# Kernel optimization log

Hardware: AMD Instinct MI355X
Metric: run time of the kernel (lower is better)

Reference implementation:

```python
import jax, jax.numpy as jnp
import numpy as np

B, P, C, UP = 4, 512, 384, 4
K1, K2, KR = 16, 8, 16
NOISE_SCALE = 0.02


def setup_inputs() -> dict:
    key = jax.random.key(0)
    ks = jax.random.split(key, 32)
    w = lambda i, s: (jax.random.normal(ks[i], s, jnp.float32) * 0.02)
    return {
        "ctx_xyz": jax.random.normal(ks[0], (B, P, 3), jnp.float32),
        "ctx_tokens": jax.random.normal(ks[1], (B, P, C), jnp.float32),
        "pred_xyz": jax.random.normal(ks[2], (B, P, 3), jnp.float32),
        "pred_token": jax.random.normal(ks[3], (B, P, C), jnp.float32),
        "noise": jax.random.normal(ks[4], (B, P * UP, 3), jnp.float32),
        "conv1_w1": w(5, (2 * C, C // 2)), "conv1_b1": jnp.zeros((C // 2,), jnp.float32),
        "conv1_w2": w(6, (C // 2, C // 2)), "conv1_b2": jnp.zeros((C // 2,), jnp.float32),
        "conv2_w1": w(7, (2 * (C // 2), C // 4)), "conv2_b1": jnp.zeros((C // 4,), jnp.float32),
        "conv2_w2": w(8, (C // 4, C // 4)), "conv2_b2": jnp.zeros((C // 4,), jnp.float32),
        "cdef_w1": w(9, (C // 4, C // 4)), "cdef_b1": jnp.zeros((C // 4,), jnp.float32),
        "cdef_w2": w(10, (C // 4, 3)), "cdef_b2": jnp.zeros((3,), jnp.float32),
        "fold_w1": w(11, (C // 4 + 3, 256)), "fold_b1": jnp.zeros((256,), jnp.float32),
        "fold_w2": w(12, (256, 256)), "fold_b2": jnp.zeros((256,), jnp.float32),
        "fold_w3": w(13, (256, 3)), "fold_b3": jnp.zeros((3,), jnp.float32),
        "ref_w1": w(14, (2 * (C // 4 + 3), C)), "ref_b1": jnp.zeros((C,), jnp.float32),
        "ref_w2": w(15, (C, 3)), "ref_b2": jnp.zeros((3,), jnp.float32),
    }


def knn_idx(x, k):
    # x: [N, D]; k nearest neighbors by L2, no self-loops (as knn_graph loop=False)
    sq = jnp.sum(x * x, axis=1)
    d = sq[:, None] + sq[None, :] - 2.0 * (x @ x.T)  # [N, N]
    n = x.shape[0]
    d = d.at[jnp.arange(n), jnp.arange(n)].set(jnp.inf)
    return jax.lax.top_k(-d, k)[1]  # [N, k]


def edge_max(x, idx, mlp):
    # EdgeConv: out[i] = max_j mlp([x_i, x_j - x_i])
    n, k = idx.shape
    xi = jnp.broadcast_to(x[:, None, :], (n, k, x.shape[1]))
    xj = x[idx]  # [N, k, D]
    return jnp.max(mlp(jnp.concatenate([xi, xj - xi], axis=-1)), axis=1)


def mlp2(w1, b1, w2, b2):
    return lambda t: jnp.maximum(t @ w1 + b1, 0.0) @ w2 + b2


def reference(ctx_xyz, ctx_tokens, pred_xyz, pred_token, noise,
              conv1_w1, conv1_b1, conv1_w2, conv1_b2,
              conv2_w1, conv2_b1, conv2_w2, conv2_b2,
              cdef_w1, cdef_b1, cdef_w2, cdef_b2,
              fold_w1, fold_b1, fold_w2, fold_b2, fold_w3, fold_b3,
              ref_w1, ref_b1, ref_w2, ref_b2):
    def shared_edgeconv(x):
        h = edge_max(x, knn_idx(x, K1), mlp2(conv1_w1, conv1_b1, conv1_w2, conv1_b2))
        return edge_max(h, knn_idx(h, K2), mlp2(conv2_w1, conv2_b1, conv2_w2, conv2_b2))

    # context branch
    ctx_xyz_f = ctx_xyz.reshape(-1, 3)
    ctx_tok_f = ctx_tokens.reshape(-1, C)
    ctx_feat = shared_edgeconv(ctx_tok_f)                       # [B*P, C//4]
    ctx_xyz_out = ctx_xyz_f + 0.05 * mlp2(cdef_w1, cdef_b1, cdef_w2, cdef_b2)(ctx_feat)

    # target branch: upsample + assign tokens
    tgt_xyz = (jnp.repeat(pred_xyz, UP, axis=1) + NOISE_SCALE * noise).reshape(-1, 3)
    tgt_tok = jnp.repeat(ctx_tokens, UP, axis=1).reshape(-1, C)
    tgt_feat = shared_edgeconv(tgt_tok)                         # [B*P*UP, C//4]

    # folding MLP (Linear-ReLU-Linear-ReLU-Linear) residual
    h = jnp.concatenate([tgt_xyz, tgt_feat], axis=-1)
    h = jnp.maximum(h @ fold_w1 + fold_b1, 0.0)
    h = jnp.maximum(h @ fold_w2 + fold_b2, 0.0)
    tgt_xyz = tgt_xyz + h @ fold_w3 + fold_b3

    # GNN refiner: knn over xyz, EdgeConv over [feat, xyz]
    idx = knn_idx(tgt_xyz, KR)
    xcat = jnp.concatenate([tgt_feat, tgt_xyz], axis=-1)
    tgt_xyz = tgt_xyz + edge_max(xcat, idx, mlp2(ref_w1, ref_b1, ref_w2, ref_b2))

    return jnp.concatenate([ctx_xyz_out, tgt_xyz], axis=0)
```

## Files before the change

### kernel.cpp

```cpp
#include <hip/hip_runtime.h>

#define N2 2048
#define N8 8192
#define CDIM 384
#define H1C 192
#define H2C 96
#define PDIM 512
#define KRR 16
#define FOLDH 256
#define XCAP 256
#define XTILE 1024
#define INFF 3.0e38f

__device__ __forceinline__ float frelu(float x) { return x > 0.f ? x : 0.f; }

__device__ __forceinline__ void bitonic64_val(float& d, int lane) {
    #pragma unroll
    for (int k = 2; k <= 64; k <<= 1) {
        #pragma unroll
        for (int j = k >> 1; j > 0; j >>= 1) {
            float od = __shfl_xor(d, j);
            bool lower = (lane & j) == 0;
            bool olt = od < d;
            bool take = lower ? olt : !olt;
            if (lane & k) take = !take;
            if (take) d = od;
        }
    }
}

__device__ __forceinline__ void bitonic64_pair(float& d, int& c, int lane) {
    #pragma unroll
    for (int k = 2; k <= 64; k <<= 1) {
        #pragma unroll
        for (int j = k >> 1; j > 0; j >>= 1) {
            float od = __shfl_xor(d, j);
            int   oc = __shfl_xor(c, j);
            bool lower = (lane & j) == 0;
            bool olt = (od < d) || (od == d && oc < c);
            bool take = lower ? olt : !olt;
            if (lane & k) take = !take;
            if (take) { d = od; c = oc; }
        }
    }
}

__device__ __forceinline__ void select_slow(const float* bd, const int* bi, int cnt,
                                            int ksel, int row, int n, int* out, int lane) {
    float cd[4]; int cix[4];
    #pragma unroll
    for (int s = 0; s < 4; ++s) {
        int c = lane + 64*s;
        bool v = c < cnt;
        cd[s]  = v ? bd[c] : INFF;
        cix[s] = v ? bi[c] : 0x7fffffff;
    }
    for (int r = 0; r < ksel; ++r) {
        float lv = cd[0]; int li = cix[0];
        #pragma unroll
        for (int s = 1; s < 4; ++s) {
            if (cd[s] < lv || (cd[s] == lv && cix[s] < li)) { lv = cd[s]; li = cix[s]; }
        }
        float wv = lv; int wi = li;
        #pragma unroll
        for (int s = 1; s < 64; s <<= 1) {
            float ov = __shfl_xor(wv, s); int oi = __shfl_xor(wi, s);
            if (ov < wv || (ov == wv && oi < wi)) { wv = ov; wi = oi; }
        }
        if (lane == 0) {
            int safe = ((unsigned)wi < (unsigned)n) ? wi : ((row + 1) & (n - 1));
            out[row*ksel + r] = safe;
        }
        #pragma unroll
        for (int s = 0; s < 4; ++s) {
            if (cd[s] == wv && cix[s] == wi) { cd[s] = INFF; cix[s] = 0x7fffffff; }
        }
    }
}

__global__ __launch_bounds__(256) void rowsq_kernel(const float* __restrict__ x,
                                                    float* __restrict__ sq, int d) {
    int wave = threadIdx.x >> 6, lane = threadIdx.x & 63;
    int row = blockIdx.x*4 + wave;
    float acc = 0.f;
    for (int k = lane; k < d; k += 64) { float v = x[(size_t)row*d + k]; acc += v*v; }
    #pragma unroll
    for (int s = 1; s < 64; s <<= 1) acc += __shfl_xor(acc, s);
    if (lane == 0) sq[row] = acc;
}

__device__ __forceinline__ void disttri_body(const float* __restrict__ x, const float* __restrict__ sq,
                                             float* __restrict__ dist, int n, int K) {
    int l = blockIdx.x;
    int by = (int)((sqrtf(8.f*(float)l + 1.f) - 1.f)*0.5f);
    while ((by+1)*(by+2)/2 <= l) ++by;
    while (by*(by+1)/2 > l) --by;
    int bx = l - by*(by+1)/2;
    int row0 = by*64, col0 = bx*64;
    __shared__ __align__(16) float As[16][68];
    __shared__ __align__(16) float Bs[16][68];
    __shared__ __align__(16) float T[64][68];
    int tx = threadIdx.x, ty = threadIdx.y;
    int t = ty*16 + tx;
    float acc[4][4] = {};
    for (int k0 = 0; k0 < K; k0 += 16) {
        #pragma unroll
        for (int r = 0; r < 4; ++r) {
            int e = t + 256*r; int kk = e & 15, mm = e >> 4;
            As[kk][mm] = x[(size_t)(row0+mm)*K + k0+kk];
            Bs[kk][mm] = x[(size_t)(col0+mm)*K + k0+kk];
        }
        __syncthreads();
        #pragma unroll
        for (int kk = 0; kk < 16; ++kk) {
            float4 a4 = *(const float4*)&As[kk][ty*4];
            float4 b4 = *(const float4*)&Bs[kk][tx*4];
            acc[0][0] += a4.x*b4.x; acc[0][1] += a4.x*b4.y; acc[0][2] += a4.x*b4.z; acc[0][3] += a4.x*b4.w;
            acc[1][0] += a4.y*b4.x; acc[1][1] += a4.y*b4.y; acc[1][2] += a4.y*b4.z; acc[1][3] += a4.y*b4.w;
            acc[2][0] += a4.z*b4.x; acc[2][1] += a4.z*b4.y; acc[2][2] += a4.z*b4.z; acc[2][3] += a4.z*b4.w;
            acc[3][0] += a4.w*b4.x; acc[3][1] += a4.w*b4.y; acc[3][2] += a4.w*b4.z; acc[3][3] += a4.w*b4.w;
        }
        __syncthreads();
    }
    bool mirror = (row0 != col0);
    #pragma unroll
    for (int i2 = 0; i2 < 4; ++i2) {
        int row = row0 + ty*4 + i2;
        float sr = sq[row];
        float4 o;
        o.x = sr + sq[col0+tx*4+0] - 2.f*acc[i2][0];
        o.y = sr + sq[col0+tx*4+1] - 2.f*acc[i2][1];
        o.z = sr + sq[col0+tx*4+2] - 2.f*acc[i2][2];
        o.w = sr + sq[col0+tx*4+3] - 2.f*acc[i2][3];
        *(float4*)&dist[(size_t)row*n + col0 + tx*4] = o;
        if (mirror) {
            T[tx*4+0][ty*4+i2] = o.x;
            T[tx*4+1][ty*4+i2] = o.y;
            T[tx*4+2][ty*4+i2] = o.z;
            T[tx*4+3][ty*4+i2] = o.w;
        }
    }
    if (mirror) {
        __syncthreads();
        #pragma unroll
        for (int i2 = 0; i2 < 4; ++i2) {
            int orow = col0 + ty*4 + i2;
            float4 o = *(const float4*)&T[ty*4+i2][tx*4];
            *(float4*)&dist[(size_t)orow*n + row0 + tx*4] = o;
        }
    }
}

__global__ __launch_bounds__(256) void dist64tri_kernel(const float* __restrict__ x,
                                                        const float* __restrict__ sq,
                                                        float* __restrict__ dist, int n, int K) {
    disttri_body(x, sq, dist, n, K);
}

__global__ __launch_bounds__(256) void distpairtri_kernel(const float* __restrict__ xA,
                                                          const float* __restrict__ sqA,
                                                          float* __restrict__ dA,
                                                          const float* __restrict__ xB,
                                                          const float* __restrict__ sqB,
                                                          float* __restrict__ dB, int n, int K) {
    const float* x  = blockIdx.z ? xB : xA;
    const float* sq = blockIdx.z ? sqB : sqA;
    float* dist     = blockIdx.z ? dB : dA;
    disttri_body(x, sq, dist, n, K);
}

__device__ __forceinline__ void gemm_body(const float* __restrict__ A, const float* __restrict__ Bw,
                                          const float* __restrict__ BwB, const float* __restrict__ bias,
                                          float* __restrict__ C, int m, int K) {
    __shared__ __align__(16) float As[16][68];
    __shared__ __align__(16) float Bs[16][68];
    int tx = threadIdx.x, ty = threadIdx.y;
    int t = ty*16 + tx;
    int row0 = blockIdx.y*64, col0 = blockIdx.x*64;
    float acc[4][4] = {};
    for (int k0 = 0; k0 < K; k0 += 16) {
        #pragma unroll
        for (int r = 0; r < 4; ++r) {
            int e = t + 256*r; int kk = e & 15, mm = e >> 4;
            As[kk][mm] = (k0 + kk < K) ? A[(size_t)(row0+mm)*K + k0+kk] : 0.f;
        }
        #pragma unroll
        for (int r = 0; r < 4; ++r) {
            int e = t + 256*r; int nn = e & 63, kk = e >> 6;
            int col = col0 + nn, k = k0 + kk;
            float bv = 0.f;
            if (k < K && col < m) {
                bv = Bw[(size_t)k*m + col];
                if (BwB) bv -= BwB[(size_t)k*m + col];
            }
            Bs[kk][nn] = bv;
        }
        __syncthreads();
        #pragma unroll
        for (int kk = 0; kk < 16; ++kk) {
            float4 a4 = *(const float4*)&As[kk][ty*4];
            float4 b4 = *(const float4*)&Bs[kk][tx*4];
            acc[0][0] += a4.x*b4.x; acc[0][1] += a4.x*b4.y; acc[0][2] += a4.x*b4.z; acc[0][3] += a4.x*b4.w;
            acc[1][0] += a4.y*b4.x; acc[1][1] += a4.y*b4.y; acc[1][2] += a4.y*b4.z; acc[1][3] += a4.y*b4.w;
            acc[2][0] += a4.z*b4.x; acc[2][1] += a4.z*b4.y; acc[2][2] += a4.z*b4.z; acc[2][3] += a4.z*b4.w;
            acc[3][0] += a4.w*b4.x; acc[3][1] += a4.w*b4.y; acc[3][2] += a4.w*b4.z; acc[3][3] += a4.w*b4.w;
        }
        __syncthreads();
    }
    #pragma unroll
    for (int i2 = 0; i2 < 4; ++i2) {
        int row = row0 + ty*4 + i2;
        #pragma unroll
        for (int j2 = 0; j2 < 4; ++j2) {
            int col = col0 + tx*4 + j2;
            if (col < m) C[(size_t)row*m + col] = acc[i2][j2] + (bias ? bias[col] : 0.f);
        }
    }
}

__global__ __launch_bounds__(256) void gemmquad_kernel(
    const float* A0, const float* Bw0, const float* BwB0, const float* bias0, float* C0,
    const float* A1, const float* Bw1, const float* BwB1, const float* bias1, float* C1,
    const float* A2, const float* Bw2, const float* BwB2, const float* bias2, float* C2,
    const float* A3, const float* Bw3, const float* BwB3, const float* bias3, float* C3,
    int m, int K) {
    int z = blockIdx.z;
    const float* A    = (z==0)?A0 :(z==1)?A1 :(z==2)?A2 :A3;
    const float* Bw   = (z==0)?Bw0:(z==1)?Bw1:(z==2)?Bw2:Bw3;
    const float* BwB  = (z==0)?BwB0:(z==1)?BwB1:(z==2)?BwB2:BwB3;
    const float* bias = (z==0)?bias0:(z==1)?bias1:(z==2)?bias2:bias3;
    float* C          = (z==0)?C0 :(z==1)?C1 :(z==2)?C2 :C3;
    gemm_body(A, Bw, BwB, bias, C, m, K);
}

template<int ETOT, int SELF, int IDXS, int YT>
__device__ __forceinline__ void edge_gemm_body(const float* __restrict__ u, const float* __restrict__ v,
                                               const int* __restrict__ idx,
                                               const float* __restrict__ Bw, const float* __restrict__ bias,
                                               float* __restrict__ O, int m, int K, int npts) {
    if ((int)blockIdx.y >= YT) return;
    __shared__ __align__(16) float As[16][68];
    __shared__ __align__(16) float Bs[16][68];
    int tx = threadIdx.x, ty = threadIdx.y;
    int t = ty*16 + tx;
    int row0 = blockIdx.y*64, col0 = blockIdx.x*64;
    float acc[4][4] = {};
    for (int k0 = 0; k0 < K; k0 += 16) {
        #pragma unroll
        for (int r = 0; r < 4; ++r) {
            int e_ = t + 256*r; int kk = e_ & 15, mm = e_ >> 4;
            int row = row0 + mm, k = k0 + kk;
            int i = row / ETOT;
            int e = row - i*ETOT;
            int j = (SELF && e == 0) ? i : idx[i*IDXS + (e - SELF)];
            j = ((unsigned)j < (unsigned)npts) ? j : i;
            As[kk][mm] = frelu(u[(size_t)i*K + k] + v[(size_t)j*K + k]);
        }
        #pragma unroll
        for (int r = 0; r < 4; ++r) {
            int e_ = t + 256*r; int nn = e_ & 63, kk = e_ >> 6;
            Bs[kk][nn] = Bw[(size_t)(k0+kk)*m + col0 + nn];
        }
        __syncthreads();
        #pragma unroll
        for (int kk = 0; kk < 16; ++kk) {
            float4 a4 = *(const float4*)&As[kk][ty*4];
            float4 b4 = *(const float4*)&Bs[kk][tx*4];
            acc[0][0] += a4.x*b4.x; acc[0][1] += a4.x*b4.y; acc[0][2] += a4.x*b4.z; acc[0][3] += a4.x*b4.w;
            acc[1][0] += a4.y*b4.x; acc[1][1] += a4.y*b4.y; acc[1][2] += a4.y*b4.z; acc[1][3] += a4.y*b4.w;
            acc[2][0] += a4.z*b4.x; acc[2][1] += a4.z*b4.y; acc[2][2] += a4.z*b4.z; acc[2][3] += a4.z*b4.w;
            acc[3][0] += a4.w*b4.x; acc[3][1] += a4.w*b4.y; acc[3][2] += a4.w*b4.z; acc[3][3] += a4.w*b4.w;
        }
        __syncthreads();
    }
    #pragma unroll
    for (int i2 = 0; i2 < 4; ++i2) {
        int row = row0 + ty*4 + i2;
        #pragma unroll
        for (int j2 = 0; j2 < 4; ++j2) {
            int col = col0 + tx*4 + j2;
            O[(size_t)row*m + col] = acc[i2][j2] + bias[col];
        }
    }
}

__global__ __launch_bounds__(256) void edge_gemm1_kernel(const float* u1, const float* v1,
                                                         const int* cidx1,
                                                         const float* Bw, const float* bias,
                                                         float* Octx, float* Otgt, int npts) {
    if (blockIdx.z == 0) edge_gemm_body<16,0,16,512>(u1, v1, cidx1, Bw, bias, Octx, H1C, H1C, npts);
    else                 edge_gemm_body<5,1,16,160>(u1, v1, cidx1, Bw, bias, Otgt, H1C, H1C, npts);
}

__global__ __launch_bounds__(256) void edge_gemm2_kernel(const float* u2c, const float* v2c,
                                                         const float* u2t, const float* v2t,
                                                         const int* cidx2, const int* tidx2,
                                                         const float* Bw, const float* bias,
                                                         float* Octx, float* Otgt, int npts) {
    if (blockIdx.z == 0) edge_gemm_body<8,0,8,256>(u2c, v2c, cidx2, Bw, bias, Octx, H2C, H2C, npts);
    else                 edge_gemm_body<3,1,2,96>(u2t, v2t, tidx2, Bw, bias, Otgt, H2C, H2C, npts);
}

__global__ __launch_bounds__(192) void reduce1_kernel(const float* __restrict__ O1c,
                                                      const float* __restrict__ O1t,
                                                      float* __restrict__ h_ctx, float* __restrict__ sq_c,
                                                      float* __restrict__ h_tgt, float* __restrict__ sq_t) {
    int i = blockIdx.x, tid = threadIdx.x, wave = tid >> 6, lane = tid & 63;
    __shared__ float pm[3];
    const float* O = blockIdx.y ? O1t : O1c;
    float* h   = blockIdx.y ? h_tgt : h_ctx;
    float* sqo = blockIdx.y ? sq_t : sq_c;
    int E = blockIdx.y ? 5 : 16;
    const float* base = O + (size_t)i*E*H1C + tid;
    float best = base[0];
    for (int e = 1; e < E; ++e) best = fmaxf(best, base[(size_t)e*H1C]);
    h[(size_t)i*H1C + tid] = best;
    float part = best*best;
    #pragma unroll
    for (int s = 1; s < 64; s <<= 1) part += __shfl_xor(part, s);
    if (lane == 0) pm[wave] = part;
    __syncthreads();
    if (tid == 0) sqo[i] = pm[0] + pm[1] + pm[2];
}

__global__ __launch_bounds__(128) void reduce2_kernel(const float* __restrict__ O2c,
                                                      const float* __restrict__ O2t,
                                                      const float* __restrict__ cdw1, const float* __restrict__ cdb1,
                                                      const float* __restrict__ cdw2, const float* __restrict__ cdb2,
                                                      const float* __restrict__ ctx_xyz,
                                                      float* __restrict__ out_ctx, float* __restrict__ tfeat) {
    int i = blockIdx.x, tid = threadIdx.x, wave = tid >> 6, lane = tid & 63;
    __shared__ float sf_[96], st2_[96];
    if (blockIdx.y == 1) {
        if (tid < 96) {
            const float* base = O2t + (size_t)i*3*H2C + tid;
            float best = fmaxf(fmaxf(base[0], base[H2C]), base[2*H2C]);
            tfeat[(size_t)i*H2C + tid] = best;
        }
        return;
    }
    if (tid < 96) {
        const float* base = O2c + (size_t)i*8*H2C + tid;
        float best = base[0];
        #pragma unroll
        for (int e = 1; e < 8; ++e) best = fmaxf(best, base[(size_t)e*H2C]);
        sf_[tid] = best;
    }
    __syncthreads();
    if (tid < 96) {
        float a = cdb1[tid];
        for (int k = 0; k < 96; ++k) a += sf_[k]*cdw1[k*96 + tid];
        st2_[tid] = frelu(a);
    }
    __syncthreads();
    if (wave == 0) {
        float s0 = st2_[lane];
        float p0 = s0*cdw2[lane*3+0], p1 = s0*cdw2[lane*3+1], p2 = s0*cdw2[lane*3+2];
        if (lane < 32) {
            float s1 = st2_[lane+64];
            p0 += s1*cdw2[(lane+64)*3+0];
            p1 += s1*cdw2[(lane+64)*3+1];
            p2 += s1*cdw2[(lane+64)*3+2];
        }
        #pragma unroll
        for (int s = 1; s < 64; s <<= 1) {
            p0 += __shfl_xor(p0, s); p1 += __shfl_xor(p1, s); p2 += __shfl_xor(p2, s);
        }
        if (lane == 0) {
            out_ctx[i*3+0] = ctx_xyz[i*3+0] + 0.05f*(cdb2[0] + p0);
            out_ctx[i*3+1] = ctx_xyz[i*3+1] + 0.05f*(cdb2[1] + p1);
            out_ctx[i*3+2] = ctx_xyz[i*3+2] + 0.05f*(cdb2[2] + p2);
        }
    }
}

__global__ __launch_bounds__(256) void gatherpair_kernel(
    const float* __restrict__ featd, const float* __restrict__ xyzg,
    const float* Bw0, const float* BwB0, const float* bias0, float* C0,
    const float* Bw1, const float* BwB1, const float* bias1, float* C1,
    int m, int K) {
    int z = blockIdx.z;
    const float* Bw   = z ? Bw1 : Bw0;
    const float* BwB  = z ? BwB1 : BwB0;
    const float* bias = z ? bias1 : bias0;
    float* C          = z ? C1 : C0;
    __shared__ __align__(16) float As[16][68];
    __shared__ __align__(16) float Bs[16][68];
    int tx = threadIdx.x, ty = threadIdx.y;
    int t = ty*16 + tx;
    int row0 = blockIdx.y*64, col0 = blockIdx.x*64;
    float acc[4][4] = {};
    for (int k0 = 0; k0 < K; k0 += 16) {
        #pragma unroll
        for (int r = 0; r < 4; ++r) {
            int e = t + 256*r; int kk = e & 15, mm = e >> 4;
            int k = k0 + kk, grow = row0 + mm;
            float av = 0.f;
            if (k < K) {
                if (k < 96) { int b = grow >> 11, p = (grow & 2047) >> 2;
                              av = featd[(size_t)(b*PDIM + p)*H2C + k]; }
                else av = xyzg[(size_t)grow*3 + (k - 96)];
            }
            As[kk][mm] = av;
        }
        #pragma unroll
        for (int r = 0; r < 4; ++r) {
            int e = t + 256*r; int nn = e & 63, kk = e >> 6;
            int col = col0 + nn, k = k0 + kk;
            float bv = 0.f;
            if (k < K && col < m) {
                bv = Bw[(size_t)k*m + col];
                if (BwB) bv -= BwB[(size_t)k*m + col];
            }
            Bs[kk][nn] = bv;
        }
        __syncthreads();
        #pragma unroll
        for (int kk = 0; kk < 16; ++kk) {
            float4 a4 = *(const float4*)&As[kk][ty*4];
            float4 b4 = *(const float4*)&Bs[kk][tx*4];
            acc[0][0] += a4.x*b4.x; acc[0][1] += a4.x*b4.y; acc[0][2] += a4.x*b4.z; acc[0][3] += a4.x*b4.w;
            acc[1][0] += a4.y*b4.x; acc[1][1] += a4.y*b4.y; acc[1][2] += a4.y*b4.z; acc[1][3] += a4.y*b4.w;
            acc[2][0] += a4.z*b4.x; acc[2][1] += a4.z*b4.y; acc[2][2] += a4.z*b4.z; acc[2][3] += a4.z*b4.w;
            acc[3][0] += a4.w*b4.x; acc[3][1] += a4.w*b4.y; acc[3][2] += a4.w*b4.z; acc[3][3] += a4.w*b4.w;
        }
        __syncthreads();
    }
    #pragma unroll
    for (int i2 = 0; i2 < 4; ++i2) {
        int row = row0 + ty*4 + i2;
        #pragma unroll
        for (int j2 = 0; j2 < 4; ++j2) {
            int col = col0 + tx*4 + j2;
            if (col < m) C[(size_t)row*m + col] = acc[i2][j2] + (bias ? bias[col] : 0.f);
        }
    }
}

__global__ __launch_bounds__(256) void knn_dist_rt_kernel(const float* __restrict__ dA,
                                                          const float* __restrict__ dB, int n,
                                                          int* __restrict__ outA, int* __restrict__ outB,
                                                          int kA, int kB, int nblkA) {
    int wave = threadIdx.x >> 6, lane = threadIdx.x & 63;
    bool useB = (int)blockIdx.x >= nblkA;
    const float* dist = useB ? dB : dA;
    int* out = useB ? outB : outA;
    int ksel = useB ? kB : kA;
    int bx = useB ? (int)blockIdx.x - nblkA : (int)blockIdx.x;
    int row = bx*4 + wave;
    __shared__ float bufd[4][XCAP];
    __shared__ int   bufi[4][XCAP];
    __shared__ int   lcnt[4];
    const float4* drow = (const float4*)(dist + (size_t)row*n);
    int nq = n >> 2;
    float mv = INFF;
    for (int i = lane; i < nq; i += 64) {
        float4 d4 = drow[i]; int base = i*4;
        float a = (base+0 == row) ? INFF : d4.x;
        float b = (base+1 == row) ? INFF : d4.y;
        float c = (base+2 == row) ? INFF : d4.z;
        float d = (base+3 == row) ? INFF : d4.w;
        mv = fminf(mv, fminf(fminf(a,b), fminf(c,d)));
    }
    float sd = mv;
    bitonic64_val(sd, lane);
    float Tv = __shfl(sd, ksel - 1);
    if (lane == 0) lcnt[wave] = 0;
    for (int i = lane; i < nq; i += 64) {
        float4 d4 = drow[i]; int base = i*4;
        float dv4[4] = {d4.x, d4.y, d4.z, d4.w};
        #pragma unroll
        for (int q = 0; q < 4; ++q) {
            int col = base + q;
            if (col != row && dv4[q] <= Tv) {
                int pos = atomicAdd(&lcnt[wave], 1);
                if (pos < XCAP) { bufd[wave][pos] = dv4[q]; bufi[wave][pos] = col; }
            }
        }
    }
    int cnt = lcnt[wave]; if (cnt > XCAP) cnt = XCAP;
    if (cnt <= 64) {
        float d = (lane < cnt) ? bufd[wave][lane] : INFF;
        int   c = (lane < cnt) ? bufi[wave][lane] : 0x7fffffff;
        bitonic64_pair(d, c, lane);
        if (lane < ksel) {
            int safe = ((unsigned)c < (unsigned)n) ? c : ((row + 1) & (n - 1));
            out[row*ksel + lane] = safe;
        }
    } else {
        select_slow(bufd[wave], bufi[wave], cnt, ksel, row, n, out, lane);
    }
}

__global__ __launch_bounds__(256) void knn_xyz8_kernel(const float4* __restrict__ pts, int n,
                                                       int* __restrict__ out_idx) {
    int tid = threadIdx.x, wave = tid >> 6, lane = tid & 63;
    int rbase = blockIdx.x*8 + wave*2;
    __shared__ __align__(16) float4 tile[XTILE];
    __shared__ float bufd[8][XCAP];
    __shared__ int   bufi[8][XCAP];
    __shared__ int   lcnt[8];
    float4 P0 = pts[rbase], P1 = pts[rbase + 1];
    float mv0 = INFF, mv1 = INFF;
    for (int t0 = 0; t0 < n; t0 += XTILE) {
        __syncthreads();
        #pragma unroll
        for (int k = 0; k < XTILE/256; ++k) tile[tid + 256*k] = pts[t0 + tid + 256*k];
        __syncthreads();
        for (int c = lane; c < XTILE; c += 64) {
            float4 q = tile[c];
            int col = t0 + c;
            float d0 = P0.w + q.w - 2.f*(P0.x*q.x + P0.y*q.y + P0.z*q.z);
            float d1 = P1.w + q.w - 2.f*(P1.x*q.x + P1.y*q.y + P1.z*q.z);
            d0 = (col == rbase)     ? INFF : d0;
            d1 = (col == rbase + 1) ? INFF : d1;
            mv0 = fminf(mv0, d0);
            mv1 = fminf(mv1, d1);
        }
    }
    float s0 = mv0, s1 = mv1;
    bitonic64_val(s0, lane);
    bitonic64_val(s1, lane);
    float Tv0 = __shfl(s0, 15);
    float Tv1 = __shfl(s1, 15);
    if (lane < 2) lcnt[wave*2 + lane] = 0;
    for (int t0 = 0; t0 < n; t0 += XTILE) {
        __syncthreads();
        #pragma unroll
        for (int k = 0; k < XTILE/256; ++k) tile[tid + 256*k] = pts[t0 + tid + 256*k];
        __syncthreads();
        for (int c = lane; c < XTILE; c += 64) {
            float4 q = tile[c];
            int col = t0 + c;
            float d0 = P0.w + q.w - 2.f*(P0.x*q.x + P0.y*q.y + P0.z*q.z);
            float d1 = P1.w + q.w - 2.f*(P1.x*q.x + P1.y*q.y + P1.z*q.z);
            if (col != rbase && d0 <= Tv0) {
                int pos = atomicAdd(&lcnt[wave*2], 1);
                if (pos < XCAP) { bufd[wave*2][pos] = d0; bufi[wave*2][pos] = col; }
            }
            if (col != rbase + 1 && d1 <= Tv1) {
                int pos = atomicAdd(&lcnt[wave*2 + 1], 1);
                if (pos < XCAP) { bufd[wave*2 + 1][pos] = d1; bufi[wave*2 + 1][pos] = col; }
            }
        }
    }
    for (int jj = 0; jj < 2; ++jj) {
        int brow = wave*2 + jj, row = rbase + jj;
        int cnt = lcnt[brow]; if (cnt > XCAP) cnt = XCAP;
        if (cnt <= 64) {
            float d = (lane < cnt) ? bufd[brow][lane] : INFF;
            int   c = (lane < cnt) ? bufi[brow][lane] : 0x7fffffff;
            bitonic64_pair(d, c, lane);
            if (lane < 16) {
                int safe = ((unsigned)c < (unsigned)n) ? c : ((row + 1) & (n - 1));
                out_idx[row*16 + lane] = safe;
            }
        } else {
            select_slow(bufd[brow], bufi[brow], cnt, 16, row, n, out_idx, lane);
        }
    }
}

__global__ __launch_bounds__(256) void edge_ref_kernel(const float* __restrict__ ur,
                                                       const float* __restrict__ vr,
                                                       const float* __restrict__ w2,
                                                       const float* __restrict__ b2,
                                                       const int* __restrict__ idx,
                                                       const float* __restrict__ xyz_in,
                                                       float* __restrict__ out, int n) {
    int wave = threadIdx.x >> 6, lane = threadIdx.x & 63;
    int i = blockIdx.x*4 + wave;
    if (i >= n) return;
    float m0 = -INFF, m1 = -INFF, m2 = -INFF;
    float uh[6];
    #pragma unroll
    for (int t = 0; t < 6; ++t) uh[t] = ur[(size_t)i*384 + lane + 64*t];
    for (int e = 0; e < KRR; ++e) {
        int j = idx[i*KRR + e];
        j = ((unsigned)j < (unsigned)n) ? j : i;
        float a0 = 0.f, a1 = 0.f, a2 = 0.f;
        #pragma unroll
        for (int t = 0; t < 6; ++t) {
            int h = lane + 64*t;
            float tv = frelu(uh[t] + vr[(size_t)j*384 + h]);
            a0 += tv*w2[h*3+0]; a1 += tv*w2[h*3+1]; a2 += tv*w2[h*3+2];
        }
        #pragma unroll
        for (int s = 32; s > 0; s >>= 1) {
            a0 += __shfl_xor(a0, s); a1 += __shfl_xor(a1, s); a2 += __shfl_xor(a2, s);
        }
        m0 = fmaxf(m0, a0 + b2[0]); m1 = fmaxf(m1, a1 + b2[1]); m2 = fmaxf(m2, a2 + b2[2]);
    }
    if (lane == 0) {
        out[i*3+0] = xyz_in[i*3+0] + m0;
        out[i*3+1] = xyz_in[i*3+1] + m1;
        out[i*3+2] = xyz_in[i*3+2] + m2;
    }
}

__global__ __launch_bounds__(256) void fold_kernel(const float* __restrict__ pred_xyz,
                                                   const float* __restrict__ noise,
                                                   const float* __restrict__ featd,
                                                   const float* __restrict__ w1, const float* __restrict__ b1,
                                                   const float* __restrict__ w2, const float* __restrict__ b2,
                                                   const float* __restrict__ w3, const float* __restrict__ b3,
                                                   float* __restrict__ xyz1, float4* __restrict__ pts_out) {
    const int PTS = 16;
    int base = blockIdx.x * PTS;
    int tid = threadIdx.x;
    __shared__ __align__(16) float xin[PTS][100];
    __shared__ __align__(16) float h1[PTS][FOLDH];
    __shared__ __align__(16) float h2s[PTS][FOLDH];
    __shared__ float oxyz[PTS][3];
    for (int t = tid; t < PTS*100; t += 256) {
        int pt = t/100, k = t - pt*100;
        int gi = base + pt;
        float vv = 0.f;
        if (k < 3) {
            int b = gi >> 11, p = (gi & 2047) >> 2;
            vv = pred_xyz[(size_t)(b*PDIM + p)*3 + k] + 0.02f*noise[(size_t)gi*3 + k];
        } else if (k < 99) {
            int b = gi >> 11, p = (gi & 2047) >> 2;
            vv = featd[(size_t)(b*PDIM + p)*H2C + (k - 3)];
        }
        xin[pt][k] = vv;
    }
    __syncthreads();
    int c = tid;
    float acc[PTS];
    #pragma unroll
    for (int pt = 0; pt < PTS; ++pt) acc[pt] = b1[c];
    for (int k0 = 0; k0 < 96; k0 += 4) {
        float wa = w1[(k0+0)*FOLDH + c], wb = w1[(k0+1)*FOLDH + c];
        float wc = w1[(k0+2)*FOLDH + c], wd = w1[(k0+3)*FOLDH + c];
        #pragma unroll
        for (int pt = 0; pt < PTS; ++pt) {
            float4 xv = *(const float4*)&xin[pt][k0];
            acc[pt] += xv.x*wa + xv.y*wb + xv.z*wc + xv.w*wd;
        }
    }
    {
        float wa = w1[96*FOLDH + c], wb = w1[97*FOLDH + c], wc = w1[98*FOLDH + c];
        #pragma unroll
        for (int pt = 0; pt < PTS; ++pt) {
            float4 xv = *(const float4*)&xin[pt][96];
            acc[pt] += xv.x*wa + xv.y*wb + xv.z*wc;
        }
    }
    #pragma unroll
    for (int pt = 0; pt < PTS; ++pt) h1[pt][c] = frelu(acc[pt]);
    __syncthreads();
    #pragma unroll
    for (int pt = 0; pt < PTS; ++pt) acc[pt] = b2[c];
    for (int k0 = 0; k0 < FOLDH; k0 += 4) {
        float wa = w2[(k0+0)*FOLDH + c], wb = w2[(k0+1)*FOLDH + c];
        float wc = w2[(k0+2)*FOLDH + c], wd = w2[(k0+3)*FOLDH + c];
        #pragma unroll
        for (int pt = 0; pt < PTS; ++pt) {
            float4 hv = *(const float4*)&h1[pt][k0];
            acc[pt] += hv.x*wa + hv.y*wb + hv.z*wc + hv.w*wd;
        }
    }
    #pragma unroll
    for (int pt = 0; pt < PTS; ++pt) h2s[pt][c] = frelu(acc[pt]);
    __syncthreads();
    if (tid < PTS*3) {
        int pt = tid/3, cc = tid - pt*3;
        float a = b3[cc];
        for (int k0 = 0; k0 < FOLDH; k0 += 4) {
            float4 hv = *(const float4*)&h2s[pt][k0];
            a += hv.x*w3[(k0+0)*3+cc] + hv.y*w3[(k0+1)*3+cc] + hv.z*w3[(k0+2)*3+cc] + hv.w*w3[(k0+3)*3+cc];
        }
        int gi = base + pt;
        float res = xin[pt][cc] + a;
        xyz1[(size_t)gi*3 + cc] = res;
        oxyz[pt][cc] = res;
    }
    __syncthreads();
    if (tid < PTS) {
        float x = oxyz[tid][0], y = oxyz[tid][1], z = oxyz[tid][2];
        pts_out[base + tid] = make_float4(x, y, z, x*x + y*y + z*z);
    }
}

extern "C" void kernel_launch(void* const* d_in, const int* in_sizes, int n_in,
                              void* d_out, int out_size, void* d_ws, size_t ws_size,
                              hipStream_t stream) {
    const float* ctx_xyz    = (const float*)d_in[0];
    const float* ctx_tokens = (const float*)d_in[1];
    const float* pred_xyz   = (const float*)d_in[2];
    const float* noise      = (const float*)d_in[4];
    const float* c1w1 = (const float*)d_in[5];
    const float* c1b1 = (const float*)d_in[6];
    const float* c1w2 = (const float*)d_in[7];
    const float* c1b2 = (const float*)d_in[8];
    const float* c2w1 = (const float*)d_in[9];
    const float* c2b1 = (const float*)d_in[10];
    const float* c2w2 = (const float*)d_in[11];
    const float* c2b2 = (const float*)d_in[12];
    const float* cdw1 = (const float*)d_in[13];
    const float* cdb1 = (const float*)d_in[14];
    const float* cdw2 = (const float*)d_in[15];
    const float* cdb2 = (const float*)d_in[16];
    const float* fw1  = (const float*)d_in[17];
    const float* fb1  = (const float*)d_in[18];
    const float* fw2  = (const float*)d_in[19];
    const float* fb2  = (const float*)d_in[20];
    const float* fw3  = (const float*)d_in[21];
    const float* fb3  = (const float*)d_in[22];
    const float* rw1  = (const float*)d_in[23];
    const float* rb1  = (const float*)d_in[24];
    const float* rw2  = (const float*)d_in[25];
    const float* rb2  = (const float*)d_in[26];

    float* W = (float*)d_ws;
    float* dist  = W;
    float* distB = W + 4194304;
    float* O1ctx = W;
    float* O1tgt = W + 6291456;
    float* O2ctx = W;
    float* O2tgt = W + 1572864;
    float* ur    = W;
    float* vr    = W + 3145728;
    float* h_ctx = W + 8388608;
    float* h_tgt = h_ctx + 393216;
    float* UV    = h_tgt + 393216;
    float* u1  = UV;            float* v1  = UV + 393216;
    float* u2c = UV;            float* v2c = UV + 196608;
    float* u2t = UV + 393216;   float* v2t = UV + 589824;
    float* tfeat = UV + 786432;
    float* xyz1  = tfeat + 196608;
    float4* pts  = (float4*)(xyz1 + 24576);
    float* sqb     = (float*)pts + 32768;
    float* sq_hctx = sqb + N2;
    float* sq_htgt = sq_hctx + N2;
    int* cidx1 = (int*)(sq_htgt + N2);
    int* cidx2 = cidx1 + N2*16;
    int* tidx2 = cidx2 + N2*8;
    int* ridx  = tidx2 + N2*2;

    float* out_ctx = (float*)d_out;
    float* out_tgt = out_ctx + N2*3;

    dim3 b16(16, 16);
    const int NTRI = 32*33/2;
    const float* NUL = nullptr;

    rowsq_kernel<<<N2/4, 256, 0, stream>>>(ctx_tokens, sqb, CDIM);
    dist64tri_kernel<<<NTRI, b16, 0, stream>>>(ctx_tokens, sqb, dist, N2, CDIM);
    knn_dist_rt_kernel<<<N2/4, 256, 0, stream>>>(dist, dist, N2, cidx1, cidx1, 16, 16, N2/4);

    gemmquad_kernel<<<dim3(3, 32, 2), b16, 0, stream>>>(
        ctx_tokens, c1w1, c1w1 + 384*192, c1b1, u1,
        ctx_tokens, c1w1 + 384*192, NUL, NUL, v1,
        ctx_tokens, c1w1, NUL, NUL, u1,
        ctx_tokens, c1w1, NUL, NUL, v1,
        H1C, CDIM);
    edge_gemm1_kernel<<<dim3(3, 512, 2), b16, 0, stream>>>(u1, v1, cidx1, c1w2, c1b2,
                                                           O1ctx, O1tgt, N2);
    reduce1_kernel<<<dim3(N2, 2), 192, 0, stream>>>(O1ctx, O1tgt, h_ctx, sq_hctx, h_tgt, sq_htgt);

    distpairtri_kernel<<<dim3(NTRI, 1, 2), b16, 0, stream>>>(h_ctx, sq_hctx, dist,
                                                             h_tgt, sq_htgt, distB, N2, H1C);
    knn_dist_rt_kernel<<<2*(N2/4), 256, 0, stream>>>(dist, distB, N2, cidx2, tidx2, 8, 2, N2/4);
    gemmquad_kernel<<<dim3(2, 32, 4), b16, 0, stream>>>(
        h_ctx, c2w1, c2w1 + 192*96, c2b1, u2c,
        h_ctx, c2w1 + 192*96, NUL, NUL, v2c,
        h_tgt, c2w1, c2w1 + 192*96, c2b1, u2t,
        h_tgt, c2w1 + 192*96, NUL, NUL, v2t,
        H2C, H1C);

    edge_gemm2_kernel<<<dim3(2, 256, 2), b16, 0, stream>>>(u2c, v2c, u2t, v2t, cidx2, tidx2,
                                                           c2w2, c2b2, O2ctx, O2tgt, N2);
    reduce2_kernel<<<dim3(N2, 2), 128, 0, stream>>>(O2ctx, O2tgt, cdw1, cdb1, cdw2, cdb2,
                                                    ctx_xyz, out_ctx, tfeat);

    fold_kernel<<<N8/16, 256, 0, stream>>>(pred_xyz, noise, tfeat, fw1, fb1, fw2, fb2, fw3, fb3, xyz1, pts);

    knn_xyz8_kernel<<<N8/8, 256, 0, stream>>>(pts, N8, ridx);

    gatherpair_kernel<<<dim3(6, N8/64, 2), b16, 0, stream>>>(
        tfeat, xyz1,
        rw1, rw1 + 99*384, rb1, ur,
        rw1 + 99*384, NUL, NUL, vr,
        384, 99);
    edge_ref_kernel<<<N8/4, 256, 0, stream>>>(ur, vr, rw2, rb2, ridx, xyz1, out_tgt, N8);
}
```

Before: 453.8 us.

## Fuse EdgeConv max-reduction into edge GEMM epilogue and widen xyz kNN rows

The edge GEMM kernels now reduce the per-edge outputs to a per-point max in shared memory and write features directly, instead of storing the full per-edge matrices and running separate reduce kernels. The edge dimension is padded to a power of two, with padded edges repeating the self point, so the max stays correct. Row norms are then computed by a separate paired rowsq kernel, and a thin cdef kernel handles the context deformation. Separately, the xyz kNN kernel handles four rows per wave instead of two to reuse each loaded tile across more queries. The padding adds wasted GEMM work on the target branch (5→8, 3→4 edges), and the larger kNN kernel uses more shared memory and registers.

```diff
diff --git a/kernel.cpp b/kernel.cpp
--- a/kernel.cpp
+++ b/kernel.cpp
@@ -80,6 +80,21 @@
 
 __global__ __launch_bounds__(256) void rowsq_kernel(const float* __restrict__ x,
                                                     float* __restrict__ sq, int d) {
+    int wave = threadIdx.x >> 6, lane = threadIdx.x & 63;
+    int row = blockIdx.x*4 + wave;
+    float acc = 0.f;
+    for (int k = lane; k < d; k += 64) { float v = x[(size_t)row*d + k]; acc += v*v; }
+    #pragma unroll
+    for (int s = 1; s < 64; s <<= 1) acc += __shfl_xor(acc, s);
+    if (lane == 0) sq[row] = acc;
+}
+
+__global__ __launch_bounds__(256) void rowsqpair_kernel(const float* __restrict__ xA,
+                                                        float* __restrict__ sqA,
+                                                        const float* __restrict__ xB,
+                                                        float* __restrict__ sqB, int d) {
+    const float* x = blockIdx.y ? xB : xA;
+    float* sq = blockIdx.y ? sqB : sqA;
     int wave = threadIdx.x >> 6, lane = threadIdx.x & 63;
     int row = blockIdx.x*4 + wave;
     float acc = 0.f;
@@ -233,14 +248,17 @@
     gemm_body(A, Bw, BwB, bias, C, m, K);
 }
 
-template<int ETOT, int SELF, int IDXS, int YT>
-__device__ __forceinline__ void edge_gemm_body(const float* __restrict__ u, const float* __restrict__ v,
-                                               const int* __restrict__ idx,
-                                               const float* __restrict__ Bw, const float* __restrict__ bias,
-                                               float* __restrict__ O, int m, int K, int npts) {
+template<int EPT, int SELF, int EREAL, int IDXS, int YT>
+__device__ __forceinline__ void edge_fused_body(const float* __restrict__ u, const float* __restrict__ v,
+                                                const int* __restrict__ idx,
+                                                const float* __restrict__ Bw, const float* __restrict__ bias,
+                                                float* __restrict__ hout, int m, int K, int npts) {
     if ((int)blockIdx.y >= YT) return;
+    constexpr int LOG2EPT = (EPT == 16) ? 4 : (EPT == 8) ? 3 : 2;
+    constexpr int PPB = 64 / EPT;
     __shared__ __align__(16) float As[16][68];
     __shared__ __align__(16) float Bs[16][68];
+    __shared__ __align__(16) float Cs[64][68];
     int tx = threadIdx.x, ty = threadIdx.y;
     int t = ty*16 + tx;
     int row0 = blockIdx.y*64, col0 = blockIdx.x*64;
@@ -250,16 +268,20 @@
         for (int r = 0; r < 4; ++r) {
             int e_ = t + 256*r; int kk = e_ & 15, mm = e_ >> 4;
             int row = row0 + mm, k = k0 + kk;
-            int i = row / ETOT;
-            int e = row - i*ETOT;
-            int j = (SELF && e == 0) ? i : idx[i*IDXS + (e - SELF)];
+            int i = row >> LOG2EPT;
+            int e = row - (i << LOG2EPT);
+            int j;
+            if (SELF && e == 0) j = i;
+            else if (e < EREAL) j = idx[i*IDXS + (e - SELF)];
+            else j = i;
             j = ((unsigned)j < (unsigned)npts) ? j : i;
             As[kk][mm] = frelu(u[(size_t)i*K + k] + v[(size_t)j*K + k]);
         }
         #pragma unroll
         for (int r = 0; r < 4; ++r) {
             int e_ = t + 256*r; int nn = e_ & 63, kk = e_ >> 6;
-            Bs[kk][nn] = Bw[(size_t)(k0+kk)*m + col0 + nn];
+            int col = col0 + nn;
+            Bs[kk][nn] = (col < m) ? Bw[(size_t)(k0+kk)*m + col] : 0.f;
         }
         __syncthreads();
         #pragma unroll
@@ -275,77 +297,51 @@
     }
     #pragma unroll
     for (int i2 = 0; i2 < 4; ++i2) {
-        int row = row0 + ty*4 + i2;
         #pragma unroll
         for (int j2 = 0; j2 < 4; ++j2) {
             int col = col0 + tx*4 + j2;
-            O[(size_t)row*m + col] = acc[i2][j2] + bias[col];
-        }
-    }
-}
-
-__global__ __launch_bounds__(256) void edge_gemm1_kernel(const float* u1, const float* v1,
-                                                         const int* cidx1,
-                                                         const float* Bw, const float* bias,
-                                                         float* Octx, float* Otgt, int npts) {
-    if (blockIdx.z == 0) edge_gemm_body<16,0,16,512>(u1, v1, cidx1, Bw, bias, Octx, H1C, H1C, npts);
-    else                 edge_gemm_body<5,1,16,160>(u1, v1, cidx1, Bw, bias, Otgt, H1C, H1C, npts);
-}
-
-__global__ __launch_bounds__(256) void edge_gemm2_kernel(const float* u2c, const float* v2c,
-                                                         const float* u2t, const float* v2t,
-                                                         const int* cidx2, const int* tidx2,
-                                                         const float* Bw, const float* bias,
-                                                         float* Octx, float* Otgt, int npts) {
-    if (blockIdx.z == 0) edge_gemm_body<8,0,8,256>(u2c, v2c, cidx2, Bw, bias, Octx, H2C, H2C, npts);
-    else                 edge_gemm_body<3,1,2,96>(u2t, v2t, tidx2, Bw, bias, Otgt, H2C, H2C, npts);
-}
-
-__global__ __launch_bounds__(192) void reduce1_kernel(const float* __restrict__ O1c,
-                                                      const float* __restrict__ O1t,
-                                                      float* __restrict__ h_ctx, float* __restrict__ sq_c,
-                                                      float* __restrict__ h_tgt, float* __restrict__ sq_t) {
-    int i = blockIdx.x, tid = threadIdx.x, wave = tid >> 6, lane = tid & 63;
-    __shared__ float pm[3];
-    const float* O = blockIdx.y ? O1t : O1c;
-    float* h   = blockIdx.y ? h_tgt : h_ctx;
-    float* sqo = blockIdx.y ? sq_t : sq_c;
-    int E = blockIdx.y ? 5 : 16;
-    const float* base = O + (size_t)i*E*H1C + tid;
-    float best = base[0];
-    for (int e = 1; e < E; ++e) best = fmaxf(best, base[(size_t)e*H1C]);
-    h[(size_t)i*H1C + tid] = best;
-    float part = best*best;
-    #pragma unroll
-    for (int s = 1; s < 64; s <<= 1) part += __shfl_xor(part, s);
-    if (lane == 0) pm[wave] = part;
+            Cs[ty*4+i2][tx*4+j2] = acc[i2][j2] + ((col < m) ? bias[col] : 0.f);
+        }
+    }
     __syncthreads();
-    if (tid == 0) sqo[i] = pm[0] + pm[1] + pm[2];
-}
-
-__global__ __launch_bounds__(128) void reduce2_kernel(const float* __restrict__ O2c,
-                                                      const float* __restrict__ O2t,
-                                                      const float* __restrict__ cdw1, const float* __restrict__ cdb1,
-                                                      const float* __restrict__ cdw2, const float* __restrict__ cdb2,
-                                                      const float* __restrict__ ctx_xyz,
-                                                      float* __restrict__ out_ctx, float* __restrict__ tfeat) {
+    for (int tt = t; tt < PPB*64; tt += 256) {
+        int p = tt >> 6, c = tt & 63;
+        int col = col0 + c;
+        if (col < m) {
+            float best = Cs[p*EPT][c];
+            #pragma unroll
+            for (int e = 1; e < EPT; ++e) best = fmaxf(best, Cs[p*EPT + e][c]);
+            int i = (row0 >> LOG2EPT) + p;
+            hout[(size_t)i*m + col] = best;
+        }
+    }
+}
+
+__global__ __launch_bounds__(256) void edge_fused1_kernel(const float* u1, const float* v1,
+                                                          const int* cidx1,
+                                                          const float* Bw, const float* bias,
+                                                          float* h_ctx, float* h_tgt, int npts) {
+    if (blockIdx.z == 0) edge_fused_body<16,0,16,16,512>(u1, v1, cidx1, Bw, bias, h_ctx, H1C, H1C, npts);
+    else                 edge_fused_body<8,1,5,16,256>(u1, v1, cidx1, Bw, bias, h_tgt, H1C, H1C, npts);
+}
+
+__global__ __launch_bounds__(256) void edge_fused2_kernel(const float* u2c, const float* v2c,
+                                                          const float* u2t, const float* v2t,
+                                                          const int* cidx2, const int* tidx2,
+                                                          const float* Bw, const float* bias,
+                                                          float* cfeat, float* tfeat, int npts) {
+    if (blockIdx.z == 0) edge_fused_body<8,0,8,8,256>(u2c, v2c, cidx2, Bw, bias, cfeat, H2C, H2C, npts);
+    else                 edge_fused_body<4,1,3,2,128>(u2t, v2t, tidx2, Bw, bias, tfeat, H2C, H2C, npts);
+}
+
+__global__ __launch_bounds__(128) void cdef_kernel(const float* __restrict__ cfeat,
+                                                   const float* __restrict__ cdw1, const float* __restrict__ cdb1,
+                                                   const float* __restrict__ cdw2, const float* __restrict__ cdb2,
+                                                   const float* __restrict__ ctx_xyz,
+                                                   float* __restrict__ out_ctx) {
     int i = blockIdx.x, tid = threadIdx.x, wave = tid >> 6, lane = tid & 63;
     __shared__ float sf_[96], st2_[96];
-    if (blockIdx.y == 1) {
-        if (tid < 96) {
-            const float* base = O2t + (size_t)i*3*H2C + tid;
-            float best = fmaxf(fmaxf(base[0], base[H2C]), base[2*H2C]);
-            tfeat[(size_t)i*H2C + tid] = best;
-        }
-        return;
-    }
-    if (tid < 96) {
-        const float* base = O2c + (size_t)i*8*H2C + tid;
-        float best = base[0];
-        #pragma unroll
-        for (int e = 1; e < 8; ++e) best = fmaxf(best, base[(size_t)e*H2C]);
-        sf_[tid] = best;
-    }
+    if (tid < 96) sf_[tid] = cfeat[(size_t)i*H2C + tid];
     __syncthreads();
     if (tid < 96) {
         float a = cdb1[tid];
@@ -492,16 +488,16 @@
     }
 }
 
-__global__ __launch_bounds__(256) void knn_xyz8_kernel(const float4* __restrict__ pts, int n,
-                                                       int* __restrict__ out_idx) {
+__global__ __launch_bounds__(256) void knn_xyz16_kernel(const float4* __restrict__ pts, int n,
+                                                        int* __restrict__ out_idx) {
     int tid = threadIdx.x, wave = tid >> 6, lane = tid & 63;
-    int rbase = blockIdx.x*8 + wave*2;
+    int rbase = blockIdx.x*16 + wave*4;
     __shared__ __align__(16) float4 tile[XTILE];
-    __shared__ float bufd[8][XCAP];
-    __shared__ int   bufi[8][XCAP];
-    __shared__ int   lcnt[8];
-    float4 P0 = pts[rbase], P1 = pts[rbase + 1];
-    float mv0 = INFF, mv1 = INFF;
+    __shared__ float bufd[16][XCAP];
+    __shared__ int   bufi[16][XCAP];
+    __shared__ int   lcnt[16];
+    float4 P0 = pts[rbase], P1 = pts[rbase+1], P2 = pts[rbase+2], P3 = pts[rbase+3];
+    float mv0 = INFF, mv1 = INFF, mv2 = INFF, mv3 = INFF;
     for (int t0 = 0; t0 < n; t0 += XTILE) {
         __syncthreads();
         #pragma unroll
@@ -512,18 +508,21 @@
             int col = t0 + c;
             float d0 = P0.w + q.w - 2.f*(P0.x*q.x + P0.y*q.y + P0.z*q.z);
             float d1 = P1.w + q.w - 2.f*(P1.x*q.x + P1.y*q.y + P1.z*q.z);
-            d0 = (col == rbase)     ? INFF : d0;
-            d1 = (col == rbase + 1) ? INFF : d1;
-            mv0 = fminf(mv0, d0);
-            mv1 = fminf(mv1, d1);
-        }
-    }
-    float s0 = mv0, s1 = mv1;
-    bitonic64_val(s0, lane);
-    bitonic64_val(s1, lane);
-    float Tv0 = __shfl(s0, 15);
-    float Tv1 = __shfl(s1, 15);
-    if (lane < 2) lcnt[wave*2 + lane] = 0;
+            float d2 = P2.w + q.w - 2.f*(P2.x*q.x + P2.y*q.y + P2.z*q.z);
+            float d3 = P3.w + q.w - 2.f*(P3.x*q.x + P3.y*q.y + P3.z*q.z);
+            d0 = (col == rbase)   ? INFF : d0;
+            d1 = (col == rbase+1) ? INFF : d1;
+            d2 = (col == rbase+2) ? INFF : d2;
+            d3 = (col == rbase+3) ? INFF : d3;
+            mv0 = fminf(mv0, d0); mv1 = fminf(mv1, d1);
+            mv2 = fminf(mv2, d2); mv3 = fminf(mv3, d3);
+        }
+    }
+    bitonic64_val(mv0, lane); bitonic64_val(mv1, lane);
+    bitonic64_val(mv2, lane); bitonic64_val(mv3, lane);
+    float Tv0 = __shfl(mv0, 15), Tv1 = __shfl(mv1, 15);
+    float Tv2 = __shfl(mv2, 15), Tv3 = __shfl(mv3, 15);
+    if (lane < 4) lcnt[wave*4 + lane] = 0;
     for (int t0 = 0; t0 < n; t0 += XTILE) {
         __syncthreads();
         #pragma unroll
@@ -534,18 +533,28 @@
             int col = t0 + c;
             float d0 = P0.w + q.w - 2.f*(P0.x*q.x + P0.y*q.y + P0.z*q.z);
             float d1 = P1.w + q.w - 2.f*(P1.x*q.x + P1.y*q.y + P1.z*q.z);
+            float d2 = P2.w + q.w - 2.f*(P2.x*q.x + P2.y*q.y + P2.z*q.z);
+            float d3 = P3.w + q.w - 2.f*(P3.x*q.x + P3.y*q.y + P3.z*q.z);
             if (col != rbase && d0 <= Tv0) {
-                int pos = atomicAdd(&lcnt[wave*2], 1);
-                if (pos < XCAP) { bufd[wave*2][pos] = d0; bufi[wave*2][pos] = col; }
-            }
-            if (col != rbase + 1 && d1 <= Tv1) {
-                int pos = atomicAdd(&lcnt[wave*2 + 1], 1);
-                if (pos < XCAP) { bufd[wave*2 + 1][pos] = d1; bufi[wave*2 + 1][pos] = col; }
-            }
-        }
-    }
-    for (int jj = 0; jj < 2; ++jj) {
-        int brow = wave*2 + jj, row = rbase + jj;
+                int pos = atomicAdd(&lcnt[wave*4+0], 1);
+                if (pos < XCAP) { bufd[wave*4+0][pos] = d0; bufi[wave*4+0][pos] = col; }
+            }
+            if (col != rbase+1 && d1 <= Tv1) {
+                int pos = atomicAdd(&lcnt[wave*4+1], 1);
+                if (pos < XCAP) { bufd[wave*4+1][pos] = d1; bufi[wave*4+1][pos] = col; }
+            }
+            if (col != rbase+2 && d2 <= Tv2) {
+                int pos = atomicAdd(&lcnt[wave*4+2], 1);
+                if (pos < XCAP) { bufd[wave*4+2][pos] = d2; bufi[wave*4+2][pos] = col; }
+            }
+            if (col != rbase+3 && d3 <= Tv3) {
+                int pos = atomicAdd(&lcnt[wave*4+3], 1);
+                if (pos < XCAP) { bufd[wave*4+3][pos] = d3; bufi[wave*4+3][pos] = col; }
+            }
+        }
+    }
+    for (int jj = 0; jj < 4; ++jj) {
+        int brow = wave*4 + jj, row = rbase + jj;
         int cnt = lcnt[brow]; if (cnt > XCAP) cnt = XCAP;
         if (cnt <= 64) {
             float d = (lane < cnt) ? bufd[brow][lane] : INFF;
@@ -716,10 +725,7 @@
     float* W = (float*)d_ws;
     float* dist  = W;
     float* distB = W + 4194304;
-    float* O1ctx = W;
-    float* O1tgt = W + 6291456;
-    float* O2ctx = W;
-    float* O2tgt = W + 1572864;
+    float* cfeat = W;
     float* ur    = W;
     float* vr    = W + 3145728;
     float* h_ctx = W + 8388608;
@@ -756,9 +762,9 @@
         ctx_tokens, c1w1, NUL, NUL, u1,
         ctx_tokens, c1w1, NUL, NUL, v1,
         H1C, CDIM);
-    edge_gemm1_kernel<<<dim3(3, 512, 2), b16, 0, stream>>>(u1, v1, cidx1, c1w2, c1b2,
-                                                           O1ctx, O1tgt, N2);
-    reduce1_kernel<<<dim3(N2, 2), 192, 0, stream>>>(O1ctx, O1tgt, h_ctx, sq_hctx, h_tgt, sq_htgt);
+    edge_fused1_kernel<<<dim3(3, 512, 2), b16, 0, stream>>>(u1, v1, cidx1, c1w2, c1b2,
+                                                            h_ctx, h_tgt, N2);
+    rowsqpair_kernel<<<dim3(N2/4, 2), 256, 0, stream>>>(h_ctx, sq_hctx, h_tgt, sq_htgt, H1C);
 
     distpairtri_kernel<<<dim3(NTRI, 1, 2), b16, 0, stream>>>(h_ctx, sq_hctx, dist,
                                                              h_tgt, sq_htgt, distB, N2, H1C);
@@ -770,14 +776,13 @@
         h_tgt, c2w1 + 192*96, NUL, NUL, v2t,
         H2C, H1C);
 
-    edge_gemm2_kernel<<<dim3(2, 256, 2), b16, 0, stream>>>(u2c, v2c, u2t, v2t, cidx2, tidx2,
-                                                           c2w2, c2b2, O2ctx, O2tgt, N2);
-    reduce2_kernel<<<dim3(N2, 2), 128, 0, stream>>>(O2ctx, O2tgt, cdw1, cdb1, cdw2, cdb2,
-                                                    ctx_xyz, out_ctx, tfeat);
+    edge_fused2_kernel<<<dim3(2, 256, 2), b16, 0, stream>>>(u2c, v2c, u2t, v2t, cidx2, tidx2,
+                                                            c2w2, c2b2, cfeat, tfeat, N2);
+    cdef_kernel<<<N2, 128, 0, stream>>>(cfeat, cdw1, cdb1, cdw2, cdb2, ctx_xyz, out_ctx);
 
     fold_kernel<<<N8/16, 256, 0, stream>>>(pred_xyz, noise, tfeat, fw1, fb1, fw2, fb2, fw3, fb3, xyz1, pts);
 
-    knn_xyz8_kernel<<<N8/8, 256, 0, stream>>>(pts, N8, ridx);
+    knn_xyz16_kernel<<<N8/16, 256, 0, stream>>>(pts, N8, ridx);
 
     gatherpair_kernel<<<dim3(6, N8/64, 2), b16, 0, stream>>>(
         tfeat, xyz1,
```

Result: slower. 477.1 us (+5.1%).
